# Optimization experiments

Measured on AMD Instinct MI355X. Metric: run time of the kernel, lower is better.

The kernel has to match this reference:

```python
import jax, jax.numpy as jnp
import numpy as np

IN_FEATURES = 8192
OUT_FEATURES = 8192
CODESZ = 8
CB_SIZE = 256


def fwht(x):
    """Orthonormal Walsh-Hadamard transform along last dim (power of 2).
    Equivalent to x @ H / sqrt(n) with Sylvester Hadamard H (symmetric),
    so it implements both matmul_hadU and matmul_hadUt for K=1."""
    b, n = x.shape
    h = 2
    while h <= n:
        x = x.reshape(b, n // h, h)
        half = h // 2
        a, c = x[..., :half], x[..., half:]
        x = jnp.concatenate([a + c, a - c], axis=-1)
        h *= 2
    return x.reshape(b, n) * jnp.asarray(1.0 / np.sqrt(n), x.dtype)


def setup_inputs() -> dict:
    key = jax.random.key(0)
    ks = jax.random.split(key, 8)
    inp = jax.random.normal(ks[0], (32, 4, IN_FEATURES), dtype=jnp.float16)
    Qidxs = jax.random.randint(ks[1], (OUT_FEATURES, IN_FEATURES // CODESZ), 0, CB_SIZE, dtype=jnp.int32)
    codebook_table = jax.random.normal(ks[2], (CB_SIZE, CODESZ), dtype=jnp.float32).astype(jnp.float16)
    # positive per-column rescale (scaleWH buffer)
    scaleWH = (0.5 + jax.random.uniform(ks[3], (IN_FEATURES,), dtype=jnp.float32)).astype(jnp.float16)
    # random sign vectors SU/SV (stored as int8 +-1 in torch; used as fp16 multipliers)
    SU = jnp.where(jax.random.uniform(ks[4], (IN_FEATURES,)) < 0.5, -1.0, 1.0).astype(jnp.float16)
    SV = jnp.where(jax.random.uniform(ks[5], (OUT_FEATURES,)) < 0.5, -1.0, 1.0).astype(jnp.float16)
    Wscale = jnp.asarray(0.02, dtype=jnp.float16)
    bias = (0.01 * jax.random.normal(ks[6], (OUT_FEATURES,), dtype=jnp.float32)).astype(jnp.float16)
    return {"input": inp, "Qidxs": Qidxs, "codebook_table": codebook_table,
            "scaleWH": scaleWH, "SU": SU, "SV": SV, "Wscale": Wscale, "bias": bias}


def reference(input, Qidxs, codebook_table, scaleWH, SU, SV, Wscale, bias):
    x = input.reshape(-1, IN_FEATURES).astype(jnp.float16)
    # rescale_WH + SU sign flip, fused elementwise
    x = (x / scaleWH) * SU
    # matmul_hadUt_cuda (in_features is a power of 2 -> pure orthonormal WHT)
    x = fwht(x)
    # codebook dequant + GEMM: W_hat[o, i] = codebook[Qidxs[o, i//8], i%8] * Wscale
    W_hat = codebook_table[Qidxs].reshape(OUT_FEATURES, IN_FEATURES) * Wscale  # [out, in] fp16
    out = x @ W_hat.T  # [tokens, out]
    # matmul_hadU_cuda on output side (power of 2, no truncation needed)
    out = fwht(out)
    out = out * SV + bias
    return out.reshape(input.shape[:-1] + (OUT_FEATURES,))
```

## Files before the change

### kernel.cpp

```cpp
#include <hip/hip_runtime.h>
#include <hip/hip_bf16.h>

#define IN_F 8192
#define OUT_F 8192
#define NROWS 128
#define CB 256
#define NSL 8
#define KSLICE (IN_F / NSL)
#define NTB 128
#define QC (IN_F / 8)

using bf8   = __attribute__((ext_vector_type(8))) short;
using f32x4 = __attribute__((ext_vector_type(4))) float;

typedef const __attribute__((address_space(1))) void* as1cv;
typedef __attribute__((address_space(3))) void* as3v;

__device__ inline float bf2f(unsigned int u) {
    union { unsigned int i; float f; } v; v.i = u << 16; return v.f;
}
__device__ inline unsigned short f2bf(float f) {
    __hip_bfloat16 h = __float2bfloat16(f);
    return *reinterpret_cast<unsigned short*>(&h);
}
__device__ inline void unpack8(uint4 v, float* f) {
    f[0] = bf2f(v.x & 0xffffu); f[1] = bf2f(v.x >> 16);
    f[2] = bf2f(v.y & 0xffffu); f[3] = bf2f(v.y >> 16);
    f[4] = bf2f(v.z & 0xffffu); f[5] = bf2f(v.z >> 16);
    f[6] = bf2f(v.w & 0xffffu); f[7] = bf2f(v.w >> 16);
}

#define FWHT_SCALE 0.011048543456039806f

#define FWHT16(v)                                                         \
    _Pragma("unroll")                                                     \
    for (int hb = 0; hb < 4; ++hb) {                                      \
        const int hh = 1 << hb;                                           \
        _Pragma("unroll")                                                 \
        for (int j = 0; j < 16; ++j)                                      \
            if (!(j & hh)) {                                              \
                float a_ = v[j], b_ = v[j | hh];                          \
                v[j] = a_ + b_; v[j | hh] = a_ - b_;                      \
            }                                                             \
    }

__device__ inline void fwht4096(float* v, float* lds, int t) {
    FWHT16(v)
#pragma unroll
    for (int e = 0; e < 16; ++e) lds[e * 260 + t] = v[e];
    __syncthreads();
    {
        const int base = (t & 15) * 260 + (t >> 4) * 16;
#pragma unroll
        for (int q = 0; q < 4; ++q) {
            float4 f = *reinterpret_cast<const float4*>(&lds[base + q * 4]);
            v[q * 4 + 0] = f.x; v[q * 4 + 1] = f.y;
            v[q * 4 + 2] = f.z; v[q * 4 + 3] = f.w;
        }
    }
    FWHT16(v)
    __syncthreads();
    {
        const int e = t & 15, ub = t >> 4;
#pragma unroll
        for (int i = 0; i < 16; ++i) lds[e * 260 + i * 16 + ub] = v[i];
    }
    __syncthreads();
    {
        const int e = t & 15, i = t >> 4;
#pragma unroll
        for (int ub = 0; ub < 16; ++ub) v[ub] = lds[e * 260 + i * 16 + ub];
    }
    FWHT16(v)
    __syncthreads();
    {
        const int e = t & 15, i = t >> 4;
#pragma unroll
        for (int ub = 0; ub < 16; ++ub) lds[ub * 260 + i * 16 + e] = v[ub];
    }
    __syncthreads();
    {
        const int base = (t >> 4) * 260 + (t & 15) * 16;
#pragma unroll
        for (int q = 0; q < 4; ++q) {
            float4 f = *reinterpret_cast<const float4*>(&lds[base + q * 4]);
            v[q * 4 + 0] = f.x; v[q * 4 + 1] = f.y;
            v[q * 4 + 2] = f.z; v[q * 4 + 3] = f.w;
        }
    }
}

__global__ __launch_bounds__(256) void k_pre4(const float* __restrict__ in,
                                              const float* __restrict__ scaleWH,
                                              const float* __restrict__ SU,
                                              unsigned short* __restrict__ xt) {
    __shared__ float lds[4160];
    const int r = blockIdx.x, h = blockIdx.y, t = threadIdx.x;
    float v[16];
    const float4* xp = reinterpret_cast<const float4*>(in + (size_t)r * IN_F);
    const float4* sp = reinterpret_cast<const float4*>(scaleWH);
    const float4* up = reinterpret_cast<const float4*>(SU);
#pragma unroll
    for (int q = 0; q < 4; ++q) {
        float4 xl = xp[t * 4 + q],        sl = sp[t * 4 + q],        ul = up[t * 4 + q];
        float4 xh = xp[1024 + t * 4 + q], sh = sp[1024 + t * 4 + q], uh = up[1024 + t * 4 + q];
        float lo0 = xl.x / sl.x * ul.x, hi0 = xh.x / sh.x * uh.x;
        float lo1 = xl.y / sl.y * ul.y, hi1 = xh.y / sh.y * uh.y;
        float lo2 = xl.z / sl.z * ul.z, hi2 = xh.z / sh.z * uh.z;
        float lo3 = xl.w / sl.w * ul.w, hi3 = xh.w / sh.w * uh.w;
        v[q * 4 + 0] = h ? lo0 - hi0 : lo0 + hi0;
        v[q * 4 + 1] = h ? lo1 - hi1 : lo1 + hi1;
        v[q * 4 + 2] = h ? lo2 - hi2 : lo2 + hi2;
        v[q * 4 + 3] = h ? lo3 - hi3 : lo3 + hi3;
    }
    fwht4096(v, lds, t);
    const int ub = t >> 4, i = t & 15;
    const int kblk = h * 128 + ub * 8 + (i >> 1);
    const size_t base = ((size_t)(r >> 4) * 256 + kblk) * 512 + (size_t)(r & 15) * 8;
#pragma unroll
    for (int half = 0; half < 2; ++half) {
        unsigned int w[4];
#pragma unroll
        for (int p = 0; p < 4; ++p) {
            unsigned int lo = f2bf(v[half * 8 + 2 * p]     * FWHT_SCALE);
            unsigned int hi = f2bf(v[half * 8 + 2 * p + 1] * FWHT_SCALE);
            w[p] = lo | (hi << 16);
        }
        const int oct = (i & 1) * 2 + half;
        *reinterpret_cast<uint4*>(xt + base + oct * 128) = make_uint4(w[0], w[1], w[2], w[3]);
    }
}

__global__ __launch_bounds__(256, 2) void k_gemm10(
        const unsigned short* __restrict__ xt,
        const int* __restrict__ Qidxs,
        const float* __restrict__ cb,
        const float* __restrict__ wscale,
        unsigned short* __restrict__ pout) {
    __shared__ __align__(16) unsigned short cbl[CB][8];
    __shared__ __align__(16) int Qlds[2][128 * 64];
    const int tid = threadIdx.x;
    const int wave = tid >> 6, lane = tid & 63;
    const int wr = wave >> 1, wc = wave & 1;
    const int lr = lane & 15, lk8 = lane >> 4;
    const int n0 = blockIdx.x * NTB;
    const int ks0 = blockIdx.y * KSLICE;
    const int ksb = ks0 >> 5;
    const int c0 = ks0 >> 3;

    auto stageQ = [&](int buf, int ch) {
#pragma unroll
        for (int j = 0; j < 8; ++j) {
            const int row = j * 16 + wave * 4 + (lane >> 4);
            const int cgs = (lane & 15) ^ (row & 15);
            const int* g = Qidxs + (size_t)(n0 + row) * QC + c0 + ch * 64 + cgs * 4;
            as3v l = (as3v)(&Qlds[buf][(j * 16 + wave * 4) * 64]);
            __builtin_amdgcn_global_load_lds((as1cv)(const void*)g, l, 16, 0, 0);
        }
    };

    stageQ(0, 0);
    const float wsc = wscale[0];
    for (int e = tid; e < CB * 8; e += 256) cbl[e >> 3][e & 7] = f2bf(cb[e] * wsc);

    f32x4 acc[4][4];
#pragma unroll
    for (int mt = 0; mt < 4; ++mt)
#pragma unroll
        for (int nt = 0; nt < 4; ++nt) acc[mt][nt] = (f32x4){0.f, 0.f, 0.f, 0.f};

    const unsigned short* xw = xt + ((size_t)(wr * 4) * 256 + ksb) * 512 + lane * 8;
    __syncthreads();
    stageQ(1, 1);

#define CHUNK(BUF, CH)                                                        \
    _Pragma("unroll")                                                         \
    for (int itc = 0; itc < 16; ++itc) {                                      \
        const int it = (CH) * 16 + itc;                                       \
        const int qcol = ((itc ^ lr) << 2) + lk8;                             \
        const int qv0 = Qlds[BUF][(wc * 64 +  0 + lr) * 64 + qcol];           \
        const int qv1 = Qlds[BUF][(wc * 64 + 16 + lr) * 64 + qcol];           \
        const int qv2 = Qlds[BUF][(wc * 64 + 32 + lr) * 64 + qcol];           \
        const int qv3 = Qlds[BUF][(wc * 64 + 48 + lr) * 64 + qcol];           \
        bf8 a0 = *reinterpret_cast<const bf8*>(xw + ((size_t)(0 * 256) + it) * 512); \
        bf8 a1 = *reinterpret_cast<const bf8*>(xw + ((size_t)(1 * 256) + it) * 512); \
        bf8 a2 = *reinterpret_cast<const bf8*>(xw + ((size_t)(2 * 256) + it) * 512); \
        bf8 a3 = *reinterpret_cast<const bf8*>(xw + ((size_t)(3 * 256) + it) * 512); \
        bf8 b0 = *(const bf8*)&cbl[qv0][0];                                   \
        bf8 b1 = *(const bf8*)&cbl[qv1][0];                                   \
        bf8 b2 = *(const bf8*)&cbl[qv2][0];                                   \
        bf8 b3 = *(const bf8*)&cbl[qv3][0];                                   \
        acc[0][0] = __builtin_amdgcn_mfma_f32_16x16x32_bf16(a0, b0, acc[0][0], 0, 0, 0); \
        acc[0][1] = __builtin_amdgcn_mfma_f32_16x16x32_bf16(a0, b1, acc[0][1], 0, 0, 0); \
        acc[0][2] = __builtin_amdgcn_mfma_f32_16x16x32_bf16(a0, b2, acc[0][2], 0, 0, 0); \
        acc[0][3] = __builtin_amdgcn_mfma_f32_16x16x32_bf16(a0, b3, acc[0][3], 0, 0, 0); \
        acc[1][0] = __builtin_amdgcn_mfma_f32_16x16x32_bf16(a1, b0, acc[1][0], 0, 0, 0); \
        acc[1][1] = __builtin_amdgcn_mfma_f32_16x16x32_bf16(a1, b1, acc[1][1], 0, 0, 0); \
        acc[1][2] = __builtin_amdgcn_mfma_f32_16x16x32_bf16(a1, b2, acc[1][2], 0, 0, 0); \
        acc[1][3] = __builtin_amdgcn_mfma_f32_16x16x32_bf16(a1, b3, acc[1][3], 0, 0, 0); \
        acc[2][0] = __builtin_amdgcn_mfma_f32_16x16x32_bf16(a2, b0, acc[2][0], 0, 0, 0); \
        acc[2][1] = __builtin_amdgcn_mfma_f32_16x16x32_bf16(a2, b1, acc[2][1], 0, 0, 0); \
        acc[2][2] = __builtin_amdgcn_mfma_f32_16x16x32_bf16(a2, b2, acc[2][2], 0, 0, 0); \
        acc[2][3] = __builtin_amdgcn_mfma_f32_16x16x32_bf16(a2, b3, acc[2][3], 0, 0, 0); \
        acc[3][0] = __builtin_amdgcn_mfma_f32_16x16x32_bf16(a3, b0, acc[3][0], 0, 0, 0); \
        acc[3][1] = __builtin_amdgcn_mfma_f32_16x16x32_bf16(a3, b1, acc[3][1], 0, 0, 0); \
        acc[3][2] = __builtin_amdgcn_mfma_f32_16x16x32_bf16(a3, b2, acc[3][2], 0, 0, 0); \
        acc[3][3] = __builtin_amdgcn_mfma_f32_16x16x32_bf16(a3, b3, acc[3][3], 0, 0, 0); \
    }

    CHUNK(0, 0)
    __syncthreads();
    CHUNK(1, 1)
#undef CHUNK

    unsigned short* ps = pout + (size_t)blockIdx.y * (NROWS * OUT_F);
#pragma unroll
    for (int mt = 0; mt < 4; ++mt) {
        const int row = wr * 64 + mt * 16 + lk8 * 4;
#pragma unroll
        for (int nt = 0; nt < 4; ++nt) {
            const int col = n0 + wc * 64 + nt * 16 + lr;
#pragma unroll
            for (int r2 = 0; r2 < 4; ++r2)
                ps[(size_t)(row + r2) * OUT_F + col] = f2bf(acc[mt][nt][r2]);
        }
    }
}

__global__ __launch_bounds__(256) void k_post4(const unsigned short* __restrict__ pin,
                                               const float* __restrict__ SV,
                                               const float* __restrict__ bias,
                                               float* __restrict__ out) {
    __shared__ float lds[4160];
    const int r = blockIdx.x, h = blockIdx.y, t = threadIdx.x;
    float lo[16], hi[16], v[16];
#pragma unroll
    for (int j = 0; j < 16; ++j) { lo[j] = 0.f; hi[j] = 0.f; }
#pragma unroll 1
    for (int sl = 0; sl < NSL; ++sl) {
        const uint4* pl = reinterpret_cast<const uint4*>(
            pin + (size_t)sl * NROWS * OUT_F + (size_t)r * OUT_F + t * 16);
        const uint4* ph = reinterpret_cast<const uint4*>(
            pin + (size_t)sl * NROWS * OUT_F + (size_t)r * OUT_F + 4096 + t * 16);
        float a[8], b[8];
        unpack8(pl[0], a); unpack8(pl[1], b);
#pragma unroll
        for (int j = 0; j < 8; ++j) { lo[j] += a[j]; lo[8 + j] += b[j]; }
        unpack8(ph[0], a); unpack8(ph[1], b);
#pragma unroll
        for (int j = 0; j < 8; ++j) { hi[j] += a[j]; hi[8 + j] += b[j]; }
    }
#pragma unroll
    for (int j = 0; j < 16; ++j) v[j] = h ? lo[j] - hi[j] : lo[j] + hi[j];
    fwht4096(v, lds, t);
    const int cb4 = (h * 4096 + (t >> 4) * 256 + (t & 15) * 16) >> 2;
    const float4* svp = reinterpret_cast<const float4*>(SV);
    const float4* bip = reinterpret_cast<const float4*>(bias);
    float4* op = reinterpret_cast<float4*>(out + (size_t)r * OUT_F);
#pragma unroll
    for (int q = 0; q < 4; ++q) {
        float4 sv = svp[cb4 + q], bi = bip[cb4 + q], o;
        o.x = v[q * 4 + 0] * FWHT_SCALE * sv.x + bi.x;
        o.y = v[q * 4 + 1] * FWHT_SCALE * sv.y + bi.y;
        o.z = v[q * 4 + 2] * FWHT_SCALE * sv.z + bi.z;
        o.w = v[q * 4 + 3] * FWHT_SCALE * sv.w + bi.w;
        op[cb4 + q] = o;
    }
}

extern "C" void kernel_launch(void* const* d_in, const int* in_sizes, int n_in,
                              void* d_out, int out_size, void* d_ws, size_t ws_size,
                              hipStream_t stream) {
    const float* in      = (const float*)d_in[0];
    const int*   Qidxs   = (const int*)d_in[1];
    const float* cb      = (const float*)d_in[2];
    const float* scaleWH = (const float*)d_in[3];
    const float* SU      = (const float*)d_in[4];
    const float* SV      = (const float*)d_in[5];
    const float* wscale  = (const float*)d_in[6];
    const float* bias    = (const float*)d_in[7];
    float* out = (float*)d_out;

    unsigned short* xt    = (unsigned short*)d_ws;
    unsigned short* parts = (unsigned short*)((char*)d_ws
                            + (size_t)NROWS * IN_F * 2);

    k_pre4<<<dim3(NROWS, 2), 256, 0, stream>>>(in, scaleWH, SU, xt);
    k_gemm10<<<dim3(OUT_F / NTB, NSL), 256, 0, stream>>>(xt, Qidxs, cb, wscale, parts);
    k_post4<<<dim3(NROWS, 2), 256, 0, stream>>>(parts, SV, bias, out);
}
```

Measured before the change: 48.09 us.

## Restructure codebook GEMM: stage activations in LDS, pack indices to bytes, 16 K-slices

The GEMM kernel now uses 512-thread blocks with 8 waves and twice as many K slices. Each slice's activation tile is staged into LDS with global_load_lds in two phases, where before every wave read it directly from global memory. Codebook indices are loaded once, packed into bytes in LDS, and held in registers, so the per-iteration LDS index reads go away. The cost is twice as many partial-sum buffers for the post kernel to read and reduce, plus extra barriers between the staging phases.

```diff
diff --git a/kernel.cpp b/kernel.cpp
--- a/kernel.cpp
+++ b/kernel.cpp
@@ -5,8 +5,9 @@
 #define OUT_F 8192
 #define NROWS 128
 #define CB 256
-#define NSL 8
-#define KSLICE (IN_F / NSL)
+#define NSL2 16
+#define NSLT 16
+#define KSLICE2 (IN_F / NSL2)
 #define NTB 128
 #define QC (IN_F / 8)
 
@@ -131,95 +132,107 @@
     }
 }
 
-__global__ __launch_bounds__(256, 2) void k_gemm10(
+__global__ __launch_bounds__(512, 4) void k_gemm18(
         const unsigned short* __restrict__ xt,
         const int* __restrict__ Qidxs,
         const float* __restrict__ cb,
         const float* __restrict__ wscale,
         unsigned short* __restrict__ pout) {
     __shared__ __align__(16) unsigned short cbl[CB][8];
-    __shared__ __align__(16) int Qlds[2][128 * 64];
+    __shared__ __align__(16) unsigned short Al[32768];
+    __shared__ __align__(16) unsigned int Qb[128 * 16];
     const int tid = threadIdx.x;
     const int wave = tid >> 6, lane = tid & 63;
-    const int wr = wave >> 1, wc = wave & 1;
+    const int mgrp = wave & 1, ngrp = wave >> 1;
     const int lr = lane & 15, lk8 = lane >> 4;
     const int n0 = blockIdx.x * NTB;
-    const int ks0 = blockIdx.y * KSLICE;
+    const int ks0 = blockIdx.y * KSLICE2;
     const int ksb = ks0 >> 5;
     const int c0 = ks0 >> 3;
 
-    auto stageQ = [&](int buf, int ch) {
+    auto stageA = [&](int p) {
 #pragma unroll
         for (int j = 0; j < 8; ++j) {
-            const int row = j * 16 + wave * 4 + (lane >> 4);
-            const int cgs = (lane & 15) ^ (row & 15);
-            const int* g = Qidxs + (size_t)(n0 + row) * QC + c0 + ch * 64 + cgs * 4;
-            as3v l = (as3v)(&Qlds[buf][(j * 16 + wave * 4) * 64]);
+            const unsigned short* g = xt
+                + ((size_t)(wave * 256 + ksb + p * 8 + j)) * 512 + lane * 8;
+            as3v l = (as3v)(Al + (wave * 8 + j) * 512);
             __builtin_amdgcn_global_load_lds((as1cv)(const void*)g, l, 16, 0, 0);
         }
     };
 
-    stageQ(0, 0);
+    {
+        const int row = tid >> 2, qq = tid & 3;
+        const int* g = Qidxs + (size_t)(n0 + row) * QC + c0 + qq * 16;
+        int qv[16];
+#pragma unroll
+        for (int j4 = 0; j4 < 4; ++j4) {
+            int4 vv = *reinterpret_cast<const int4*>(g + j4 * 4);
+            qv[j4 * 4 + 0] = vv.x; qv[j4 * 4 + 1] = vv.y;
+            qv[j4 * 4 + 2] = vv.z; qv[j4 * 4 + 3] = vv.w;
+        }
+#pragma unroll
+        for (int m3 = 0; m3 < 4; ++m3) {
+            unsigned int D = (unsigned int)(qv[m3] & 255)
+                           | ((unsigned int)(qv[m3 + 4] & 255) << 8)
+                           | ((unsigned int)(qv[m3 + 8] & 255) << 16)
+                           | ((unsigned int)(qv[m3 + 12] & 255) << 24);
+            Qb[row * 16 + m3 * 4 + (qq >> 1) * 2 + (qq & 1)] = D;
+        }
+    }
+    stageA(0);
     const float wsc = wscale[0];
-    for (int e = tid; e < CB * 8; e += 256) cbl[e >> 3][e & 7] = f2bf(cb[e] * wsc);
-
-    f32x4 acc[4][4];
+    for (int e = tid; e < CB * 8; e += 512) cbl[e >> 3][e & 7] = f2bf(cb[e] * wsc);
+
+    f32x4 acc[4][2];
 #pragma unroll
     for (int mt = 0; mt < 4; ++mt)
 #pragma unroll
-        for (int nt = 0; nt < 4; ++nt) acc[mt][nt] = (f32x4){0.f, 0.f, 0.f, 0.f};
-
-    const unsigned short* xw = xt + ((size_t)(wr * 4) * 256 + ksb) * 512 + lane * 8;
-    __syncthreads();
-    stageQ(1, 1);
-
-#define CHUNK(BUF, CH)                                                        \
+        for (int nt = 0; nt < 2; ++nt) acc[mt][nt] = (f32x4){0.f, 0.f, 0.f, 0.f};
+
+    __syncthreads();
+
+    unsigned int qr[2][4];
+#pragma unroll
+    for (int nb = 0; nb < 2; ++nb) {
+        const int qrow = ngrp * 32 + nb * 16 + lr;
+#pragma unroll
+        for (int d = 0; d < 4; ++d) qr[nb][d] = Qb[qrow * 16 + lk8 * 4 + d];
+    }
+
+#define PHASE(PH)                                                             \
     _Pragma("unroll")                                                         \
-    for (int itc = 0; itc < 16; ++itc) {                                      \
-        const int it = (CH) * 16 + itc;                                       \
-        const int qcol = ((itc ^ lr) << 2) + lk8;                             \
-        const int qv0 = Qlds[BUF][(wc * 64 +  0 + lr) * 64 + qcol];           \
-        const int qv1 = Qlds[BUF][(wc * 64 + 16 + lr) * 64 + qcol];           \
-        const int qv2 = Qlds[BUF][(wc * 64 + 32 + lr) * 64 + qcol];           \
-        const int qv3 = Qlds[BUF][(wc * 64 + 48 + lr) * 64 + qcol];           \
-        bf8 a0 = *reinterpret_cast<const bf8*>(xw + ((size_t)(0 * 256) + it) * 512); \
-        bf8 a1 = *reinterpret_cast<const bf8*>(xw + ((size_t)(1 * 256) + it) * 512); \
-        bf8 a2 = *reinterpret_cast<const bf8*>(xw + ((size_t)(2 * 256) + it) * 512); \
-        bf8 a3 = *reinterpret_cast<const bf8*>(xw + ((size_t)(3 * 256) + it) * 512); \
-        bf8 b0 = *(const bf8*)&cbl[qv0][0];                                   \
-        bf8 b1 = *(const bf8*)&cbl[qv1][0];                                   \
-        bf8 b2 = *(const bf8*)&cbl[qv2][0];                                   \
-        bf8 b3 = *(const bf8*)&cbl[qv3][0];                                   \
+    for (int it = 0; it < 8; ++it) {                                          \
+        const int dsel = (PH) * 2 + (it >> 2), sh = (it & 3) * 8;             \
+        bf8 b0 = *(const bf8*)&cbl[(qr[0][dsel] >> sh) & 255][0];             \
+        bf8 b1 = *(const bf8*)&cbl[(qr[1][dsel] >> sh) & 255][0];             \
+        bf8 a0 = *(const bf8*)(Al + ((mgrp * 4 + 0) * 8 + it) * 512 + lane * 8); \
+        bf8 a1 = *(const bf8*)(Al + ((mgrp * 4 + 1) * 8 + it) * 512 + lane * 8); \
+        bf8 a2 = *(const bf8*)(Al + ((mgrp * 4 + 2) * 8 + it) * 512 + lane * 8); \
+        bf8 a3 = *(const bf8*)(Al + ((mgrp * 4 + 3) * 8 + it) * 512 + lane * 8); \
         acc[0][0] = __builtin_amdgcn_mfma_f32_16x16x32_bf16(a0, b0, acc[0][0], 0, 0, 0); \
         acc[0][1] = __builtin_amdgcn_mfma_f32_16x16x32_bf16(a0, b1, acc[0][1], 0, 0, 0); \
-        acc[0][2] = __builtin_amdgcn_mfma_f32_16x16x32_bf16(a0, b2, acc[0][2], 0, 0, 0); \
-        acc[0][3] = __builtin_amdgcn_mfma_f32_16x16x32_bf16(a0, b3, acc[0][3], 0, 0, 0); \
         acc[1][0] = __builtin_amdgcn_mfma_f32_16x16x32_bf16(a1, b0, acc[1][0], 0, 0, 0); \
         acc[1][1] = __builtin_amdgcn_mfma_f32_16x16x32_bf16(a1, b1, acc[1][1], 0, 0, 0); \
-        acc[1][2] = __builtin_amdgcn_mfma_f32_16x16x32_bf16(a1, b2, acc[1][2], 0, 0, 0); \
-        acc[1][3] = __builtin_amdgcn_mfma_f32_16x16x32_bf16(a1, b3, acc[1][3], 0, 0, 0); \
         acc[2][0] = __builtin_amdgcn_mfma_f32_16x16x32_bf16(a2, b0, acc[2][0], 0, 0, 0); \
         acc[2][1] = __builtin_amdgcn_mfma_f32_16x16x32_bf16(a2, b1, acc[2][1], 0, 0, 0); \
-        acc[2][2] = __builtin_amdgcn_mfma_f32_16x16x32_bf16(a2, b2, acc[2][2], 0, 0, 0); \
-        acc[2][3] = __builtin_amdgcn_mfma_f32_16x16x32_bf16(a2, b3, acc[2][3], 0, 0, 0); \
         acc[3][0] = __builtin_amdgcn_mfma_f32_16x16x32_bf16(a3, b0, acc[3][0], 0, 0, 0); \
         acc[3][1] = __builtin_amdgcn_mfma_f32_16x16x32_bf16(a3, b1, acc[3][1], 0, 0, 0); \
-        acc[3][2] = __builtin_amdgcn_mfma_f32_16x16x32_bf16(a3, b2, acc[3][2], 0, 0, 0); \
-        acc[3][3] = __builtin_amdgcn_mfma_f32_16x16x32_bf16(a3, b3, acc[3][3], 0, 0, 0); \
-    }
-
-    CHUNK(0, 0)
-    __syncthreads();
-    CHUNK(1, 1)
-#undef CHUNK
+    }
+
+    PHASE(0)
+    __syncthreads();
+    stageA(1);
+    __syncthreads();
+    PHASE(1)
+#undef PHASE
 
     unsigned short* ps = pout + (size_t)blockIdx.y * (NROWS * OUT_F);
 #pragma unroll
     for (int mt = 0; mt < 4; ++mt) {
-        const int row = wr * 64 + mt * 16 + lk8 * 4;
-#pragma unroll
-        for (int nt = 0; nt < 4; ++nt) {
-            const int col = n0 + wc * 64 + nt * 16 + lr;
+        const int row = mgrp * 64 + mt * 16 + lk8 * 4;
+#pragma unroll
+        for (int nt = 0; nt < 2; ++nt) {
+            const int col = n0 + ngrp * 32 + nt * 16 + lr;
 #pragma unroll
             for (int r2 = 0; r2 < 4; ++r2)
                 ps[(size_t)(row + r2) * OUT_F + col] = f2bf(acc[mt][nt][r2]);
@@ -227,7 +240,7 @@
     }
 }
 
-__global__ __launch_bounds__(256) void k_post4(const unsigned short* __restrict__ pin,
+__global__ __launch_bounds__(256) void k_post5(const unsigned short* __restrict__ pin,
                                                const float* __restrict__ SV,
                                                const float* __restrict__ bias,
                                                float* __restrict__ out) {
@@ -237,7 +250,7 @@
 #pragma unroll
     for (int j = 0; j < 16; ++j) { lo[j] = 0.f; hi[j] = 0.f; }
 #pragma unroll 1
-    for (int sl = 0; sl < NSL; ++sl) {
+    for (int sl = 0; sl < NSLT; ++sl) {
         const uint4* pl = reinterpret_cast<const uint4*>(
             pin + (size_t)sl * NROWS * OUT_F + (size_t)r * OUT_F + t * 16);
         const uint4* ph = reinterpret_cast<const uint4*>(
@@ -286,6 +299,6 @@
                             + (size_t)NROWS * IN_F * 2);
 
     k_pre4<<<dim3(NROWS, 2), 256, 0, stream>>>(in, scaleWH, SU, xt);
-    k_gemm10<<<dim3(OUT_F / NTB, NSL), 256, 0, stream>>>(xt, Qidxs, cb, wscale, parts);
-    k_post4<<<dim3(NROWS, 2), 256, 0, stream>>>(parts, SV, bias, out);
-}
+    k_gemm18<<<dim3(OUT_F / NTB, NSL2), 512, 0, stream>>>(xt, Qidxs, cb, wscale, parts);
+    k_post5<<<dim3(NROWS, 2), 256, 0, stream>>>(parts, SV, bias, out);
+}
```

After: 55.18 us. 14.7% more time.
